# Performance work log

Measured on AMD Instinct MI355X. Metric: run time of the kernel, lower is better.

Reference implementation:

```python
import jax, jax.numpy as jnp
import numpy as np
import math

D_EMBED, D_K, N_HEADS = 1024, 1024, 16
D_H = D_EMBED // N_HEADS          # 64
ROT_DIM = D_H // 2                # 32, RotaryEmbedding(dim=d_h//2)
B, LQ, LK = 2, 2048, 2048


def _rope_freqs(seq_len):
    # lucidrains rotary-embedding-torch: inv_freq over half of `dim`, interleave-repeated
    inv_freq = 1.0 / (10000.0 ** (jnp.arange(0, ROT_DIM, 2, dtype=jnp.float32) / ROT_DIM))
    t = jnp.arange(seq_len, dtype=jnp.float32)
    f = t[:, None] * inv_freq[None, :]          # [S, ROT_DIM/2]
    return jnp.repeat(f, 2, axis=-1)            # [S, ROT_DIM] interleaved


def _apply_rotary(x, freqs):
    # x: [B,H,S,D_H]; rotate first ROT_DIM features, pass the rest through
    x_rot, x_pass = x[..., :ROT_DIM], x[..., ROT_DIM:]
    cos, sin = jnp.cos(freqs), jnp.sin(freqs)   # [S, ROT_DIM]
    x1, x2 = x_rot[..., 0::2], x_rot[..., 1::2]
    rotated = jnp.stack((-x2, x1), axis=-1).reshape(x_rot.shape)
    return jnp.concatenate([x_rot * cos + rotated * sin, x_pass], axis=-1)


def setup_inputs() -> dict:
    key = jax.random.key(0)
    ks = jax.random.split(key, 12)
    s = 0.02
    return {
        "embed": jax.random.normal(ks[0], (B, LQ, D_EMBED), jnp.float32),
        "key": jax.random.normal(ks[1], (B, LK, D_K), jnp.float32),
        "attn_mask": jnp.ones((B, LQ, LK), dtype=bool),
        "WQ": jax.random.normal(ks[2], (D_EMBED, D_EMBED), jnp.float32) * s,
        "bQ": jnp.zeros((D_EMBED,), jnp.float32),
        "WK": jax.random.normal(ks[3], (D_K, D_EMBED), jnp.float32) * s,
        "bK": jnp.zeros((D_EMBED,), jnp.float32),
        "WV": jax.random.normal(ks[4], (D_K, D_EMBED), jnp.float32) * s,
        "bV": jnp.zeros((D_EMBED,), jnp.float32),
        "WO": jax.random.normal(ks[5], (D_EMBED, D_EMBED), jnp.float32) * s,
        "bO": jnp.zeros((D_EMBED,), jnp.float32),
    }


def reference(embed, key, attn_mask, WQ, bQ, WK, bK, WV, bV, WO, bO):
    bsz, len_q, _ = embed.shape
    len_k = key.shape[1]
    scale = 1.0 / math.sqrt(D_EMBED)  # note: module scales by 1/sqrt(d_embed)

    Q = embed @ WQ + bQ
    K = key @ WK + bK
    V = key @ WV + bV

    # [B, H, S, D_H]
    Qh = Q.reshape(bsz, len_q, N_HEADS, D_H).transpose(0, 2, 1, 3)
    Kh = K.reshape(bsz, len_k, N_HEADS, D_H).transpose(0, 2, 1, 3)
    Vh = V.reshape(bsz, len_k, N_HEADS, D_H).transpose(0, 2, 1, 3)

    Qh = _apply_rotary(Qh, _rope_freqs(len_q))
    Kh = _apply_rotary(Kh, _rope_freqs(len_k))

    attn = jnp.einsum('bhqd,bhkd->bhqk', Qh, Kh)
    attn = jnp.where(attn_mask[:, None, :, :], attn, -jnp.inf)
    attn = jax.nn.softmax(attn * scale, axis=-1)

    out = jnp.einsum('bhqk,bhkd->bhqd', attn, Vh)
    out = out.transpose(0, 2, 1, 3).reshape(bsz, len_q, D_EMBED)
    return out @ WO + bO
```

## Files before the change

### kernel.cpp

```cpp
#include <hip/hip_runtime.h>
#include <hip/hip_bf16.h>
#include <cstdint>
#include <cstddef>

typedef __bf16 bf16_t;
typedef bf16_t bf16x8 __attribute__((ext_vector_type(8)));
typedef bf16_t bf16x4 __attribute__((ext_vector_type(4)));
typedef bf16_t bf16x2 __attribute__((ext_vector_type(2)));
typedef float f32x4 __attribute__((ext_vector_type(4)));
typedef float f32x16 __attribute__((ext_vector_type(16)));
typedef unsigned int u32x4 __attribute__((ext_vector_type(4)));

namespace {
constexpr int Bv = 2, Lv = 2048, Ev = 1024, NHv = 16;
constexpr int Mv = Bv * Lv;
constexpr float SCALE_L2E = 0.03125f * 1.4426950408889634f;
}

__device__ __forceinline__ void gload_lds16(const void* g, void* l) {
  __builtin_amdgcn_global_load_lds(
      (const __attribute__((address_space(1))) unsigned int*)g,
      (__attribute__((address_space(3))) unsigned int*)l,
      16, 0, 0);
}

__global__ __launch_bounds__(256) void k_prep(
    const float* __restrict__ embed, const float* __restrict__ key,
    bf16_t* __restrict__ Ae, bf16_t* __restrict__ Ak,
    float2* __restrict__ tab, int* __restrict__ bad,
    const unsigned int* __restrict__ m,
    const float* w0, const float* w1, const float* w2, const float* w3,
    bf16_t* t0, bf16_t* t1, bf16_t* t2, bf16_t* t3) {
  const int tid = threadIdx.x;
  int bx = blockIdx.x;
  if (bx < 8192) {
    const float* x = (bx < 4096) ? embed : key;
    bf16_t* y = (bx < 4096) ? Ae : Ak;
    int i = (bx & 4095) * 256 + tid;
    float4 v = reinterpret_cast<const float4*>(x)[i];
    bf16x4 o = {(bf16_t)v.x, (bf16_t)v.y, (bf16_t)v.z, (bf16_t)v.w};
    *reinterpret_cast<bf16x4*>(&y[(size_t)i * 4]) = o;
    return;
  }
  bx -= 8192;
  if (bx < 128) {
    int t = bx * 256 + tid;
    int i = t & 15, l = t >> 4;
    float inv = exp2f(-13.287712379549449f * (float)i * (1.0f / 16.0f));
    float s, c;
    sincosf((float)l * inv, &s, &c);
    tab[t] = make_float2(c, s);
    return;
  }
  bx -= 128;
  if (bx < 2048) {
    const int nwords = Bv * Lv * Lv;
    const int u8words = nwords >> 2;
    int i = bx * 256 + tid;
    bool badA = false, badB = false;
    for (; i < nwords; i += 2048 * 256) {
      unsigned int v = m[i];
      badA |= (i < u8words) & (v != 0x01010101u);
      badB |= (v != 1u);
    }
    if (__any(badA) && (tid & 63) == 0) bad[0] = 1;
    if (__any(badB) && (tid & 63) == 0) bad[1] = 1;
    return;
  }
  bx -= 2048;
  {
    const int z = bx >> 10, rem = bx & 1023;
    const float* W;
    bf16_t* T;
    switch (z) {
      case 0: W = w0; T = t0; break;
      case 1: W = w1; T = t1; break;
      case 2: W = w2; T = t2; break;
      default: W = w3; T = t3; break;
    }
    __shared__ float tile[32][33];
    const int tx = tid & 31, ty = tid >> 5;
    const int n0 = (rem & 31) * 32, k0 = (rem >> 5) * 32;
#pragma unroll
    for (int i = 0; i < 4; i++) {
      int r = ty + i * 8;
      tile[r][tx] = W[(size_t)(k0 + r) * Ev + n0 + tx];
    }
    __syncthreads();
#pragma unroll
    for (int i = 0; i < 4; i++) {
      int r = ty + i * 8;
      T[(size_t)(n0 + r) * Ev + k0 + tx] = (bf16_t)tile[tx][r];
    }
  }
}

__global__ __launch_bounds__(256) void k_gemm_qkv(
    const bf16_t* __restrict__ Ae, const bf16_t* __restrict__ Ak,
    const bf16_t* __restrict__ WtQ, const bf16_t* __restrict__ WtK,
    const bf16_t* __restrict__ WtV, const float* __restrict__ bQ,
    const float* __restrict__ bK, const float* __restrict__ bV,
    const float2* __restrict__ tab, bf16_t* __restrict__ Qbf,
    bf16_t* __restrict__ Kbf, bf16_t* __restrict__ Vtr) {
  constexpr int K = Ev;
  const int z = blockIdx.z;
  const bf16_t* A = (z == 0) ? Ae : Ak;
  const bf16_t* Bt = (z == 0) ? WtQ : (z == 1) ? WtK : WtV;
  const float* bias = (z == 0) ? bQ : (z == 1) ? bK : bV;

  __shared__ __align__(16) bf16_t As[128 * 32];
  __shared__ __align__(16) bf16_t Bs[128 * 32];
  const int tid = threadIdx.x;
  const int wid = tid >> 6, lane = tid & 63;
  const int bm = blockIdx.y * 128, bn = blockIdx.x * 128;
  const int wr = wid >> 1, wc = wid & 1;
  f32x4 acc[4][4] = {};
  const int srow = wid * 32 + (lane >> 2);
  const int scol = (lane & 3) * 8;
  const size_t ga0 = (size_t)(bm + srow) * K + scol;
  const size_t ga1 = (size_t)(bm + srow + 16) * K + scol;
  const size_t gb0 = (size_t)(bn + srow) * K + scol;
  const size_t gb1 = (size_t)(bn + srow + 16) * K + scol;
  bf16_t* asw = &As[wid * 1024];
  bf16_t* bsw = &Bs[wid * 1024];
  for (int k0 = 0; k0 < K; k0 += 32) {
    gload_lds16(A + ga0 + k0, asw);
    gload_lds16(A + ga1 + k0, asw + 512);
    gload_lds16(Bt + gb0 + k0, bsw);
    gload_lds16(Bt + gb1 + k0, bsw + 512);
    __syncthreads();
    bf16x8 af[4], bfr[4];
#pragma unroll
    for (int m = 0; m < 4; m++)
      af[m] = *(const bf16x8*)&As[(wr * 64 + m * 16 + (lane & 15)) * 32 + (lane >> 4) * 8];
#pragma unroll
    for (int n = 0; n < 4; n++)
      bfr[n] = *(const bf16x8*)&Bs[(wc * 64 + n * 16 + (lane & 15)) * 32 + (lane >> 4) * 8];
#pragma unroll
    for (int m = 0; m < 4; m++)
#pragma unroll
      for (int n = 0; n < 4; n++)
        acc[m][n] = __builtin_amdgcn_mfma_f32_16x16x32_bf16(af[m], bfr[n], acc[m][n], 0, 0, 0);
    __syncthreads();
  }

  const int l15 = lane & 15, g = lane >> 4;
  if (z == 2) {
#pragma unroll
    for (int n = 0; n < 4; n++) {
      const int col = bn + wc * 64 + n * 16 + l15;
      const int hh = (col >> 6) & 15;
      const int d = col & 63;
      const float bv = bias[col];
#pragma unroll
      for (int m = 0; m < 4; m++) {
        const int row0 = bm + wr * 64 + m * 16 + (g << 2);
        const int b = row0 >> 11, l0 = row0 & 2047;
        const int pq = (l0 >> 2) & 3;
        const int pq2 = ((pq & 1) << 1) | (pq >> 1);
        const int l0p = (l0 & ~12) | (pq2 << 2);
        bf16x4 ov;
#pragma unroll
        for (int r = 0; r < 4; r++) ov[r] = (bf16_t)(acc[m][n][r] + bv);
        *(bf16x4*)&Vtr[((size_t)((b * NHv + hh) * 64 + d)) * Lv + l0p] = ov;
      }
    }
    return;
  }

  bf16_t* Y = (z == 0) ? Qbf : Kbf;
  const float scale = (z == 0) ? SCALE_L2E : 1.0f;
  const float ssign = (l15 & 1) ? 1.0f : -1.0f;
#pragma unroll
  for (int n = 0; n < 4; n++) {
    const int col = bn + wc * 64 + n * 16 + l15;
    const int h = (col >> 6) & 15;
    const int d = col & 63;
    const float bv = bias[col];
    const bool dorope = (d < 32);
    const int ti = d >> 1;
#pragma unroll
    for (int m = 0; m < 4; m++) {
      const int row0 = bm + wr * 64 + m * 16 + (g << 2);
#pragma unroll
      for (int r = 0; r < 4; r++) {
        const int row = row0 + r;
        const int l = row & 2047, b = row >> 11;
        float v = acc[m][n][r] + bv;
        float p = __shfl_xor(v, 1);
        float o = v;
        if (dorope) {
          float2 cs = tab[(l << 4) + ti];
          o = v * cs.x + p * cs.y * ssign;
        }
        Y[(((size_t)(b * NHv + h)) * Lv + l) * 64 + d] = (bf16_t)(o * scale);
      }
    }
  }
}

__global__ __launch_bounds__(256) void k_gemm_bt(const bf16_t* __restrict__ A,
                                                 const bf16_t* __restrict__ Bt,
                                                 const float* __restrict__ bias,
                                                 float* __restrict__ C,
                                                 int N, int K) {
  __shared__ __align__(16) bf16_t As[128 * 32];
  __shared__ __align__(16) bf16_t Bs[64 * 32];
  const int tid = threadIdx.x;
  const int wid = tid >> 6, lane = tid & 63;
  const int bm = blockIdx.y * 128, bn = blockIdx.x * 64;
  const int wr = wid >> 1, wc = wid & 1;
  f32x4 acc[4][2] = {};
  const int srowA = wid * 32 + (lane >> 2);
  const int srowB = wid * 16 + (lane >> 2);
  const int scol = (lane & 3) * 8;
  const size_t ga0 = (size_t)(bm + srowA) * K + scol;
  const size_t ga1 = (size_t)(bm + srowA + 16) * K + scol;
  const size_t gb0 = (size_t)(bn + srowB) * K + scol;
  bf16_t* asw = &As[wid * 1024];
  bf16_t* bsw = &Bs[wid * 512];
  for (int k0 = 0; k0 < K; k0 += 32) {
    gload_lds16(A + ga0 + k0, asw);
    gload_lds16(A + ga1 + k0, asw + 512);
    gload_lds16(Bt + gb0 + k0, bsw);
    __syncthreads();
    bf16x8 af[4], bfr[2];
#pragma unroll
    for (int m = 0; m < 4; m++)
      af[m] = *(const bf16x8*)&As[(wr * 64 + m * 16 + (lane & 15)) * 32 + (lane >> 4) * 8];
#pragma unroll
    for (int n = 0; n < 2; n++)
      bfr[n] = *(const bf16x8*)&Bs[(wc * 32 + n * 16 + (lane & 15)) * 32 + (lane >> 4) * 8];
#pragma unroll
    for (int m = 0; m < 4; m++)
#pragma unroll
      for (int n = 0; n < 2; n++)
        acc[m][n] = __builtin_amdgcn_mfma_f32_16x16x32_bf16(af[m], bfr[n], acc[m][n], 0, 0, 0);
    __syncthreads();
  }
#pragma unroll
  for (int n = 0; n < 2; n++) {
    const int col = bn + wc * 32 + n * 16 + (lane & 15);
    const float bv = bias[col];
#pragma unroll
    for (int m = 0; m < 4; m++) {
      const int row0 = bm + wr * 64 + m * 16 + ((lane >> 4) << 2);
#pragma unroll
      for (int r = 0; r < 4; r++)
        C[(size_t)(row0 + r) * N + col] = acc[m][n][r] + bv;
    }
  }
}

__device__ __forceinline__ void flash_stage(const bf16_t* __restrict__ Kg,
                                            const bf16_t* __restrict__ Vg,
                                            bf16_t* ksb, bf16_t* vsb,
                                            int tid, int kt) {
#pragma unroll
  for (int i = 0; i < 2; i++) {
    int slot = i * 256 + tid;
    int r = slot >> 3, c = slot & 7;
    int sb = ((c * 16) ^ ((r & 7) << 4)) >> 1;
    bf16_t* dk = ksb + (size_t)(i * 256 + (tid & 192)) * 8;
    gload_lds16(Kg + (size_t)(kt * 64 + r) * 64 + sb, dk);
    bf16_t* dv = vsb + (size_t)(i * 256 + (tid & 192)) * 8;
    gload_lds16(Vg + (size_t)r * Lv + kt * 64 + sb, dv);
  }
}

__global__ __launch_bounds__(256) void k_flash32(const bf16_t* __restrict__ Qh,
                                                 const bf16_t* __restrict__ Kh,
                                                 const bf16_t* __restrict__ Vtr,
                                                 const int* __restrict__ mask,
                                                 const int* __restrict__ bad,
                                                 bf16_t* __restrict__ Oh) {
  __shared__ __align__(16) bf16_t Ks[2][64 * 64];
  __shared__ __align__(16) bf16_t Vs[2][64 * 64];
  __shared__ float sw[4][32];
  const int tid = threadIdx.x, wid = tid >> 6, lane = tid & 63;
  const int l31 = lane & 31, hf = lane >> 5;
  const int bh = blockIdx.x, qt = blockIdx.y;
  const int b = bh >> 4, hd = bh & 15;
  const size_t base = (size_t)bh * Lv * 64;
  const bf16_t* Kg = Kh + base;
  const bf16_t* Vg = Vtr + base;
  const int allm = !(bad[0] & bad[1]);
  const int q = qt * 128 + wid * 32 + l31;

  bf16x8 bq[4];
#pragma unroll
  for (int s = 0; s < 4; s++)
    bq[s] = *(const bf16x8*)&Qh[base + (size_t)q * 64 + s * 16 + hf * 8];

  const int xsw = (l31 & 7) << 4;
  int eo_[4];
#pragma unroll
  for (int s = 0; s < 4; s++) eo_[s] = (((s * 16 + hf * 8) * 2) ^ xsw) >> 1;

  float m_r = -INFINITY, l_p = 0.f;
  f32x16 o0 = {}, o1 = {};

  flash_stage(Kg, Vg, Ks[0], Vs[0], tid, 0);
  __syncthreads();
  int cur = 0;
  for (int kt = 0; kt < Lv / 64; ++kt) {
    if (kt + 1 < Lv / 64)
      flash_stage(Kg, Vg, Ks[cur ^ 1], Vs[cur ^ 1], tid, kt + 1);
    const bf16_t* KsC = Ks[cur];
    const bf16_t* VsC = Vs[cur];

    f32x16 st0 = {}, st1 = {};
    __builtin_amdgcn_s_setprio(1);
#pragma unroll
    for (int s = 0; s < 4; s++) {
      bf16x8 k0 = *(const bf16x8*)&KsC[l31 * 64 + eo_[s]];
      bf16x8 k1 = *(const bf16x8*)&KsC[(32 + l31) * 64 + eo_[s]];
      st0 = __builtin_amdgcn_mfma_f32_32x32x16_bf16(k0, bq[s], st0, 0, 0, 0);
      st1 = __builtin_amdgcn_mfma_f32_32x32x16_bf16(k1, bq[s], st1, 0, 0, 0);
    }
    __builtin_amdgcn_s_setprio(0);

    if (!allm) {
      const int* mrow = &mask[(size_t)b * Lv * Lv + (size_t)q * Lv + kt * 64];
#pragma unroll
      for (int r = 0; r < 16; r++) {
        const int kv = (r & 3) + 8 * (r >> 2) + 4 * hf;
        if (!mrow[kv]) st0[r] = -INFINITY;
        if (!mrow[32 + kv]) st1[r] = -INFINITY;
      }
    }

    float pm = fmaxf(st0[0], st0[1]);
#pragma unroll
    for (int r = 2; r < 16; r += 2) pm = fmaxf(fmaxf(st0[r], st0[r + 1]), pm);
#pragma unroll
    for (int r = 0; r < 16; r += 2) pm = fmaxf(fmaxf(st1[r], st1[r + 1]), pm);
    if (__any(pm > m_r + 8.0f)) {
      float pmf = fmaxf(pm, __shfl_xor(pm, 32));
      float mn = fmaxf(m_r, pmf);
      float alpha = exp2f(m_r - mn);
      m_r = mn;
      l_p *= alpha;
      if (!hf) sw[wid][l31] = alpha;
      asm volatile("s_waitcnt lgkmcnt(0)" ::: "memory");
      __builtin_amdgcn_sched_barrier(0);
#pragma unroll
      for (int r = 0; r < 16; r++) {
        float a = sw[wid][(r & 3) + 8 * (r >> 2) + 4 * hf];
        o0[r] *= a;
        o1[r] *= a;
      }
    }
    float ps = 0.f;
#pragma unroll
    for (int r = 0; r < 16; r++) {
      float p = exp2f(st0[r] - m_r);
      st0[r] = p;
      ps += p;
    }
#pragma unroll
    for (int r = 0; r < 16; r++) {
      float p = exp2f(st1[r] - m_r);
      st1[r] = p;
      ps += p;
    }
    l_p += ps;

    unsigned int pk0[8], pk1[8];
#pragma unroll
    for (int i = 0; i < 8; i++) {
      float a0 = st0[2 * i], a1 = st0[2 * i + 1];
      float b0 = st1[2 * i], b1 = st1[2 * i + 1];
      asm("v_cvt_pk_bf16_f32 %0, %1, %2" : "=v"(pk0[i]) : "v"(a0), "v"(a1));
      asm("v_cvt_pk_bf16_f32 %0, %1, %2" : "=v"(pk1[i]) : "v"(b0), "v"(b1));
    }

    __builtin_amdgcn_s_setprio(1);
#pragma unroll
    for (int s = 0; s < 4; s++) {
      u32x4 u;
      if (s == 0) {
        u[0] = pk0[0]; u[1] = pk0[1]; u[2] = pk0[2]; u[3] = pk0[3];
      } else if (s == 1) {
        u[0] = pk0[4]; u[1] = pk0[5]; u[2] = pk0[6]; u[3] = pk0[7];
      } else if (s == 2) {
        u[0] = pk1[0]; u[1] = pk1[1]; u[2] = pk1[2]; u[3] = pk1[3];
      } else {
        u[0] = pk1[4]; u[1] = pk1[5]; u[2] = pk1[6]; u[3] = pk1[7];
      }
      bf16x8 pa = __builtin_bit_cast(bf16x8, u);
      bf16x8 v0 = *(const bf16x8*)&VsC[l31 * 64 + eo_[s]];
      bf16x8 v1 = *(const bf16x8*)&VsC[(32 + l31) * 64 + eo_[s]];
      o0 = __builtin_amdgcn_mfma_f32_32x32x16_bf16(pa, v0, o0, 0, 0, 0);
      o1 = __builtin_amdgcn_mfma_f32_32x32x16_bf16(pa, v1, o1, 0, 0, 0);
    }
    __builtin_amdgcn_s_setprio(0);

    __syncthreads();
    cur ^= 1;
  }

  float lt = l_p + __shfl_xor(l_p, 32);
  if (!hf) sw[wid][l31] = 1.0f / lt;
  asm volatile("s_waitcnt lgkmcnt(0)" ::: "memory");
  __builtin_amdgcn_sched_barrier(0);
#pragma unroll
  for (int r = 0; r < 16; r++) {
    const int rq = (r & 3) + 8 * (r >> 2) + 4 * hf;
    float inv = sw[wid][rq];
    const int qg = qt * 128 + wid * 32 + rq;
    const size_t off = ((size_t)(b * Lv + qg)) * Ev + hd * 64;
    Oh[off + l31] = (bf16_t)(o0[r] * inv);
    Oh[off + 32 + l31] = (bf16_t)(o1[r] * inv);
  }
}

extern "C" void kernel_launch(void* const* d_in, const int* in_sizes, int n_in,
                              void* d_out, int out_size, void* d_ws, size_t ws_size,
                              hipStream_t stream) {
  const float* embed = (const float*)d_in[0];
  const float* key = (const float*)d_in[1];
  const int* mask = (const int*)d_in[2];
  const float* WQ = (const float*)d_in[3];
  const float* bQ = (const float*)d_in[4];
  const float* WK = (const float*)d_in[5];
  const float* bK = (const float*)d_in[6];
  const float* WV = (const float*)d_in[7];
  const float* bV = (const float*)d_in[8];
  const float* WO = (const float*)d_in[9];
  const float* bO = (const float*)d_in[10];
  float* out = (float*)d_out;
  char* ws = (char*)d_ws;
  const size_t MB = 1024 * 1024;

  bf16_t* Wt = (bf16_t*)(ws);
  bf16_t* Ae = (bf16_t*)(ws + 8 * MB);
  bf16_t* Ak = (bf16_t*)(ws + 16 * MB);
  bf16_t* Qbf = (bf16_t*)(ws + 40 * MB);
  bf16_t* Kbf = (bf16_t*)(ws + 48 * MB);
  bf16_t* Vtr = (bf16_t*)(ws + 56 * MB);
  bf16_t* AO = (bf16_t*)(ws + 8 * MB);
  int* bad = (int*)(ws + 64 * MB);
  float2* tab = (float2*)(ws + 65 * MB);

  hipMemsetAsync(bad, 0, 2 * sizeof(int), stream);
  k_prep<<<14464, 256, 0, stream>>>(embed, key, Ae, Ak, tab, bad,
                                    (const unsigned int*)mask, WQ, WK, WV, WO,
                                    Wt, Wt + 1024 * 1024, Wt + 2 * 1024 * 1024,
                                    Wt + 3 * 1024 * 1024);

  {
    dim3 gg(8, 32, 3);
    k_gemm_qkv<<<gg, 256, 0, stream>>>(Ae, Ak, Wt, Wt + 1024 * 1024,
                                       Wt + 2 * 1024 * 1024, bQ, bK, bV, tab,
                                       Qbf, Kbf, Vtr);
  }
  {
    dim3 fg(32, 16);
    k_flash32<<<fg, 256, 0, stream>>>(Qbf, Kbf, Vtr, mask, bad, AO);
  }
  {
    dim3 gg(16, 32);
    k_gemm_bt<<<gg, 256, 0, stream>>>(AO, Wt + 3 * 1024 * 1024, bO, out, Ev, Ev);
  }
}
```

Baseline: 161.9 us.

## Split flash attention over key halves with a separate combine kernel

Adds a split-K variant of the flash attention kernel. Each block processes half of the key sequence and writes unnormalized bf16 partial outputs plus per-row max and sum. A new combine kernel merges the two halves with log-sum-exp weights into the attention output. This doubles the grid to improve CU occupancy and parallelism, at the cost of extra partial-output memory traffic, an extra kernel launch, and bf16 rounding of the partials. The split path is only enabled when the workspace is large enough.

```diff
diff --git a/kernel.cpp b/kernel.cpp
--- a/kernel.cpp
+++ b/kernel.cpp
@@ -268,18 +268,22 @@
   }
 }
 
+template <bool SPLIT>
 __global__ __launch_bounds__(256) void k_flash32(const bf16_t* __restrict__ Qh,
                                                  const bf16_t* __restrict__ Kh,
                                                  const bf16_t* __restrict__ Vtr,
                                                  const int* __restrict__ mask,
                                                  const int* __restrict__ bad,
-                                                 bf16_t* __restrict__ Oh) {
+                                                 bf16_t* __restrict__ Oh,
+                                                 bf16_t* __restrict__ Opart,
+                                                 float2* __restrict__ ml) {
   __shared__ __align__(16) bf16_t Ks[2][64 * 64];
   __shared__ __align__(16) bf16_t Vs[2][64 * 64];
   __shared__ float sw[4][32];
   const int tid = threadIdx.x, wid = tid >> 6, lane = tid & 63;
   const int l31 = lane & 31, hf = lane >> 5;
   const int bh = blockIdx.x, qt = blockIdx.y;
+  const int ks = SPLIT ? blockIdx.z : 0;
   const int b = bh >> 4, hd = bh & 15;
   const size_t base = (size_t)bh * Lv * 64;
   const bf16_t* Kg = Kh + base;
@@ -300,11 +304,14 @@
   float m_r = -INFINITY, l_p = 0.f;
   f32x16 o0 = {}, o1 = {};
 
-  flash_stage(Kg, Vg, Ks[0], Vs[0], tid, 0);
+  const int kt0 = SPLIT ? ks * (Lv / 128) : 0;
+  const int kt1 = SPLIT ? kt0 + (Lv / 128) : (Lv / 64);
+
+  flash_stage(Kg, Vg, Ks[0], Vs[0], tid, kt0);
   __syncthreads();
   int cur = 0;
-  for (int kt = 0; kt < Lv / 64; ++kt) {
-    if (kt + 1 < Lv / 64)
+  for (int kt = kt0; kt < kt1; ++kt) {
+    if (kt + 1 < kt1)
       flash_stage(Kg, Vg, Ks[cur ^ 1], Vs[cur ^ 1], tid, kt + 1);
     const bf16_t* KsC = Ks[cur];
     const bf16_t* VsC = Vs[cur];
@@ -401,17 +408,55 @@
   }
 
   float lt = l_p + __shfl_xor(l_p, 32);
-  if (!hf) sw[wid][l31] = 1.0f / lt;
-  asm volatile("s_waitcnt lgkmcnt(0)" ::: "memory");
-  __builtin_amdgcn_sched_barrier(0);
-#pragma unroll
-  for (int r = 0; r < 16; r++) {
-    const int rq = (r & 3) + 8 * (r >> 2) + 4 * hf;
-    float inv = sw[wid][rq];
-    const int qg = qt * 128 + wid * 32 + rq;
-    const size_t off = ((size_t)(b * Lv + qg)) * Ev + hd * 64;
-    Oh[off + l31] = (bf16_t)(o0[r] * inv);
-    Oh[off + 32 + l31] = (bf16_t)(o1[r] * inv);
+  if (SPLIT) {
+    if (!hf) ml[((size_t)ks * 32 + bh) * Lv + q] = make_float2(m_r, lt);
+    bf16_t* po = &Opart[(((size_t)ks * 32 + bh) * Lv + qt * 128 + wid * 32) * 64];
+#pragma unroll
+    for (int r = 0; r < 16; r++) {
+      const int rq = (r & 3) + 8 * (r >> 2) + 4 * hf;
+      po[(size_t)rq * 64 + l31] = (bf16_t)o0[r];
+      po[(size_t)rq * 64 + 32 + l31] = (bf16_t)o1[r];
+    }
+  } else {
+    if (!hf) sw[wid][l31] = 1.0f / lt;
+    asm volatile("s_waitcnt lgkmcnt(0)" ::: "memory");
+    __builtin_amdgcn_sched_barrier(0);
+#pragma unroll
+    for (int r = 0; r < 16; r++) {
+      const int rq = (r & 3) + 8 * (r >> 2) + 4 * hf;
+      float inv = sw[wid][rq];
+      const int qg = qt * 128 + wid * 32 + rq;
+      const size_t off = ((size_t)(b * Lv + qg)) * Ev + hd * 64;
+      Oh[off + l31] = (bf16_t)(o0[r] * inv);
+      Oh[off + 32 + l31] = (bf16_t)(o1[r] * inv);
+    }
+  }
+}
+
+__global__ __launch_bounds__(256) void k_comb(const bf16_t* __restrict__ Opart,
+                                              const float2* __restrict__ ml,
+                                              bf16_t* __restrict__ AO) {
+  int t = blockIdx.x * 256 + threadIdx.x;
+  int q = t & (Lv - 1), bh = t >> 11;
+  float2 a = ml[(size_t)bh * Lv + q];
+  float2 c = ml[((size_t)32 + bh) * Lv + q];
+  float mx = fmaxf(a.x, c.x);
+  float e0 = exp2f(a.x - mx), e1 = exp2f(c.x - mx);
+  float denom = e0 * a.y + e1 * c.y;
+  float w0 = e0 / denom, w1 = e1 / denom;
+  const bf16_t* p0 = &Opart[((size_t)bh * Lv + q) * 64];
+  const bf16_t* p1 = &Opart[(((size_t)32 + bh) * Lv + q) * 64];
+  int b = bh >> 4, h = bh & 15;
+  bf16_t* po = &AO[((size_t)(b * Lv + q)) * Ev + h * 64];
+#pragma unroll
+  for (int cch = 0; cch < 8; cch++) {
+    bf16x8 x = *(const bf16x8*)&p0[cch * 8];
+    bf16x8 y = *(const bf16x8*)&p1[cch * 8];
+    bf16x8 o;
+#pragma unroll
+    for (int j = 0; j < 8; j++)
+      o[j] = (bf16_t)(w0 * (float)x[j] + w1 * (float)y[j]);
+    *(bf16x8*)&po[cch * 8] = o;
   }
 }
 
@@ -436,12 +481,16 @@
   bf16_t* Wt = (bf16_t*)(ws);
   bf16_t* Ae = (bf16_t*)(ws + 8 * MB);
   bf16_t* Ak = (bf16_t*)(ws + 16 * MB);
+  bf16_t* Opart = (bf16_t*)(ws + 24 * MB);
   bf16_t* Qbf = (bf16_t*)(ws + 40 * MB);
   bf16_t* Kbf = (bf16_t*)(ws + 48 * MB);
   bf16_t* Vtr = (bf16_t*)(ws + 56 * MB);
   bf16_t* AO = (bf16_t*)(ws + 8 * MB);
   int* bad = (int*)(ws + 64 * MB);
   float2* tab = (float2*)(ws + 65 * MB);
+  float2* ml = (float2*)(ws + 66 * MB);
+
+  const bool split = ws_size >= 68 * MB;
 
   hipMemsetAsync(bad, 0, 2 * sizeof(int), stream);
   k_prep<<<14464, 256, 0, stream>>>(embed, key, Ae, Ak, tab, bad,
@@ -455,9 +504,15 @@
                                        Wt + 2 * 1024 * 1024, bQ, bK, bV, tab,
                                        Qbf, Kbf, Vtr);
   }
-  {
+  if (split) {
+    dim3 fg(32, 16, 2);
+    k_flash32<true><<<fg, 256, 0, stream>>>(Qbf, Kbf, Vtr, mask, bad, AO,
+                                            Opart, ml);
+    k_comb<<<256, 256, 0, stream>>>(Opart, ml, AO);
+  } else {
     dim3 fg(32, 16);
-    k_flash32<<<fg, 256, 0, stream>>>(Qbf, Kbf, Vtr, mask, bad, AO);
+    k_flash32<false><<<fg, 256, 0, stream>>>(Qbf, Kbf, Vtr, mask, bad, AO,
+                                             Opart, ml);
   }
   {
     dim3 gg(16, 32);
```

Result: slower. 175.1 us (+8.1%).

## Software-pipeline flash attention: overlap next tile's QK/softmax with current PV

Applied to the files above, without the earlier changes.

The key loop is restructured so that QK^T, softmax and bf16 packing for tile t+1 run in the same iteration as the PV MFMAs for tile t. K/V staging moves from double to triple buffering in LDS, so the prefetch runs two tiles ahead. The output rescale for a max update is now applied after the PV of the previous tile. This is meant to hide softmax and exp latency behind matrix-core work, at the cost of more registers (two packed P arrays) and more shared memory, which may lower occupancy.

```diff
diff --git a/kernel.cpp b/kernel.cpp
--- a/kernel.cpp
+++ b/kernel.cpp
@@ -268,14 +268,76 @@
   }
 }
 
+__device__ __forceinline__ void qk_sm_pack(
+    const bf16_t* __restrict__ KsC, const bf16x8* bq, const int* eo_,
+    const int* __restrict__ mrow, int l31, int hf, float* swp,
+    float& m_r, float& l_p, bool& resc, unsigned int* pk) {
+  f32x16 st0 = {}, st1 = {};
+  __builtin_amdgcn_s_setprio(1);
+#pragma unroll
+  for (int s = 0; s < 4; s++) {
+    bf16x8 k0 = *(const bf16x8*)&KsC[l31 * 64 + eo_[s]];
+    bf16x8 k1 = *(const bf16x8*)&KsC[(32 + l31) * 64 + eo_[s]];
+    st0 = __builtin_amdgcn_mfma_f32_32x32x16_bf16(k0, bq[s], st0, 0, 0, 0);
+    st1 = __builtin_amdgcn_mfma_f32_32x32x16_bf16(k1, bq[s], st1, 0, 0, 0);
+  }
+  __builtin_amdgcn_s_setprio(0);
+
+  if (mrow) {
+#pragma unroll
+    for (int r = 0; r < 16; r++) {
+      const int kv = (r & 3) + 8 * (r >> 2) + 4 * hf;
+      if (!mrow[kv]) st0[r] = -INFINITY;
+      if (!mrow[32 + kv]) st1[r] = -INFINITY;
+    }
+  }
+
+  float pm = fmaxf(st0[0], st0[1]);
+#pragma unroll
+  for (int r = 2; r < 16; r += 2) pm = fmaxf(fmaxf(st0[r], st0[r + 1]), pm);
+#pragma unroll
+  for (int r = 0; r < 16; r += 2) pm = fmaxf(fmaxf(st1[r], st1[r + 1]), pm);
+  resc = false;
+  if (__any(pm > m_r + 8.0f)) {
+    float pmf = fmaxf(pm, __shfl_xor(pm, 32));
+    float mn = fmaxf(m_r, pmf);
+    float alpha = exp2f(m_r - mn);
+    m_r = mn;
+    l_p *= alpha;
+    if (!hf) swp[l31] = alpha;
+    resc = true;
+  }
+  float ps = 0.f;
+#pragma unroll
+  for (int r = 0; r < 16; r++) {
+    float p = exp2f(st0[r] - m_r);
+    st0[r] = p;
+    ps += p;
+  }
+#pragma unroll
+  for (int r = 0; r < 16; r++) {
+    float p = exp2f(st1[r] - m_r);
+    st1[r] = p;
+    ps += p;
+  }
+  l_p += ps;
+#pragma unroll
+  for (int i = 0; i < 8; i++) {
+    float a0 = st0[2 * i], a1 = st0[2 * i + 1];
+    float b0 = st1[2 * i], b1 = st1[2 * i + 1];
+    asm("v_cvt_pk_bf16_f32 %0, %1, %2" : "=v"(pk[i]) : "v"(a0), "v"(a1));
+    asm("v_cvt_pk_bf16_f32 %0, %1, %2" : "=v"(pk[8 + i]) : "v"(b0), "v"(b1));
+  }
+}
+
 __global__ __launch_bounds__(256) void k_flash32(const bf16_t* __restrict__ Qh,
                                                  const bf16_t* __restrict__ Kh,
                                                  const bf16_t* __restrict__ Vtr,
                                                  const int* __restrict__ mask,
                                                  const int* __restrict__ bad,
                                                  bf16_t* __restrict__ Oh) {
-  __shared__ __align__(16) bf16_t Ks[2][64 * 64];
-  __shared__ __align__(16) bf16_t Vs[2][64 * 64];
+  __shared__ __align__(16) bf16_t Ks[3][64 * 64];
+  __shared__ __align__(16) bf16_t Vs[3][64 * 64];
   __shared__ float sw[4][32];
   const int tid = threadIdx.x, wid = tid >> 6, lane = tid & 63;
   const int l31 = lane & 31, hf = lane >> 5;
@@ -284,8 +346,11 @@
   const size_t base = (size_t)bh * Lv * 64;
   const bf16_t* Kg = Kh + base;
   const bf16_t* Vg = Vtr + base;
-  const int allm = !(bad[0] & bad[1]);
+  const bool allm = !(bad[0] & bad[1]);
   const int q = qt * 128 + wid * 32 + l31;
+  const int* mbase = allm ? nullptr
+                          : &mask[(size_t)b * Lv * Lv + (size_t)q * Lv];
+  float* swp = &sw[wid][0];
 
   bf16x8 bq[4];
 #pragma unroll
@@ -299,95 +364,40 @@
 
   float m_r = -INFINITY, l_p = 0.f;
   f32x16 o0 = {}, o1 = {};
+  unsigned int pkA[16], pkB[16];
+  constexpr int NT = Lv / 64;
 
   flash_stage(Kg, Vg, Ks[0], Vs[0], tid, 0);
   __syncthreads();
-  int cur = 0;
-  for (int kt = 0; kt < Lv / 64; ++kt) {
-    if (kt + 1 < Lv / 64)
-      flash_stage(Kg, Vg, Ks[cur ^ 1], Vs[cur ^ 1], tid, kt + 1);
-    const bf16_t* KsC = Ks[cur];
-    const bf16_t* VsC = Vs[cur];
-
-    f32x16 st0 = {}, st1 = {};
-    __builtin_amdgcn_s_setprio(1);
-#pragma unroll
-    for (int s = 0; s < 4; s++) {
-      bf16x8 k0 = *(const bf16x8*)&KsC[l31 * 64 + eo_[s]];
-      bf16x8 k1 = *(const bf16x8*)&KsC[(32 + l31) * 64 + eo_[s]];
-      st0 = __builtin_amdgcn_mfma_f32_32x32x16_bf16(k0, bq[s], st0, 0, 0, 0);
-      st1 = __builtin_amdgcn_mfma_f32_32x32x16_bf16(k1, bq[s], st1, 0, 0, 0);
-    }
-    __builtin_amdgcn_s_setprio(0);
-
-    if (!allm) {
-      const int* mrow = &mask[(size_t)b * Lv * Lv + (size_t)q * Lv + kt * 64];
-#pragma unroll
-      for (int r = 0; r < 16; r++) {
-        const int kv = (r & 3) + 8 * (r >> 2) + 4 * hf;
-        if (!mrow[kv]) st0[r] = -INFINITY;
-        if (!mrow[32 + kv]) st1[r] = -INFINITY;
-      }
-    }
-
-    float pm = fmaxf(st0[0], st0[1]);
-#pragma unroll
-    for (int r = 2; r < 16; r += 2) pm = fmaxf(fmaxf(st0[r], st0[r + 1]), pm);
-#pragma unroll
-    for (int r = 0; r < 16; r += 2) pm = fmaxf(fmaxf(st1[r], st1[r + 1]), pm);
-    if (__any(pm > m_r + 8.0f)) {
-      float pmf = fmaxf(pm, __shfl_xor(pm, 32));
-      float mn = fmaxf(m_r, pmf);
-      float alpha = exp2f(m_r - mn);
-      m_r = mn;
-      l_p *= alpha;
-      if (!hf) sw[wid][l31] = alpha;
-      asm volatile("s_waitcnt lgkmcnt(0)" ::: "memory");
-      __builtin_amdgcn_sched_barrier(0);
-#pragma unroll
-      for (int r = 0; r < 16; r++) {
-        float a = sw[wid][(r & 3) + 8 * (r >> 2) + 4 * hf];
-        o0[r] *= a;
-        o1[r] *= a;
-      }
-    }
-    float ps = 0.f;
-#pragma unroll
-    for (int r = 0; r < 16; r++) {
-      float p = exp2f(st0[r] - m_r);
-      st0[r] = p;
-      ps += p;
-    }
-#pragma unroll
-    for (int r = 0; r < 16; r++) {
-      float p = exp2f(st1[r] - m_r);
-      st1[r] = p;
-      ps += p;
-    }
-    l_p += ps;
-
-    unsigned int pk0[8], pk1[8];
-#pragma unroll
-    for (int i = 0; i < 8; i++) {
-      float a0 = st0[2 * i], a1 = st0[2 * i + 1];
-      float b0 = st1[2 * i], b1 = st1[2 * i + 1];
-      asm("v_cvt_pk_bf16_f32 %0, %1, %2" : "=v"(pk0[i]) : "v"(a0), "v"(a1));
-      asm("v_cvt_pk_bf16_f32 %0, %1, %2" : "=v"(pk1[i]) : "v"(b0), "v"(b1));
-    }
-
+  flash_stage(Kg, Vg, Ks[1], Vs[1], tid, 1);
+  {
+    bool r0;
+    qk_sm_pack(Ks[0], bq, eo_, mbase ? mbase + 0 : nullptr, l31, hf, swp,
+               m_r, l_p, r0, pkA);
+  }
+  __syncthreads();
+
+  for (int t = 0; t < NT; ++t) {
+    const int bc = t % 3;
+    if (t + 2 < NT)
+      flash_stage(Kg, Vg, Ks[(t + 2) % 3], Vs[(t + 2) % 3], tid, t + 2);
+
+    bool resc = false;
+    if (t + 1 < NT) {
+      qk_sm_pack(Ks[(t + 1) % 3], bq, eo_,
+                 mbase ? mbase + (t + 1) * 64 : nullptr, l31, hf, swp,
+                 m_r, l_p, resc, pkB);
+    }
+
+    const bf16_t* VsC = Vs[bc];
     __builtin_amdgcn_s_setprio(1);
 #pragma unroll
     for (int s = 0; s < 4; s++) {
       u32x4 u;
-      if (s == 0) {
-        u[0] = pk0[0]; u[1] = pk0[1]; u[2] = pk0[2]; u[3] = pk0[3];
-      } else if (s == 1) {
-        u[0] = pk0[4]; u[1] = pk0[5]; u[2] = pk0[6]; u[3] = pk0[7];
-      } else if (s == 2) {
-        u[0] = pk1[0]; u[1] = pk1[1]; u[2] = pk1[2]; u[3] = pk1[3];
-      } else {
-        u[0] = pk1[4]; u[1] = pk1[5]; u[2] = pk1[6]; u[3] = pk1[7];
-      }
+      u[0] = pkA[4 * s + 0];
+      u[1] = pkA[4 * s + 1];
+      u[2] = pkA[4 * s + 2];
+      u[3] = pkA[4 * s + 3];
       bf16x8 pa = __builtin_bit_cast(bf16x8, u);
       bf16x8 v0 = *(const bf16x8*)&VsC[l31 * 64 + eo_[s]];
       bf16x8 v1 = *(const bf16x8*)&VsC[(32 + l31) * 64 + eo_[s]];
@@ -396,18 +406,32 @@
     }
     __builtin_amdgcn_s_setprio(0);
 
-    __syncthreads();
-    cur ^= 1;
+    if (resc) {
+      asm volatile("s_waitcnt lgkmcnt(0)" ::: "memory");
+      __builtin_amdgcn_sched_barrier(0);
+#pragma unroll
+      for (int r = 0; r < 16; r++) {
+        float a = swp[(r & 3) + 8 * (r >> 2) + 4 * hf];
+        o0[r] *= a;
+        o1[r] *= a;
+      }
+    }
+
+    __syncthreads();
+    if (t + 1 < NT) {
+#pragma unroll
+      for (int i = 0; i < 16; i++) pkA[i] = pkB[i];
+    }
   }
 
   float lt = l_p + __shfl_xor(l_p, 32);
-  if (!hf) sw[wid][l31] = 1.0f / lt;
+  if (!hf) swp[l31] = 1.0f / lt;
   asm volatile("s_waitcnt lgkmcnt(0)" ::: "memory");
   __builtin_amdgcn_sched_barrier(0);
 #pragma unroll
   for (int r = 0; r < 16; r++) {
     const int rq = (r & 3) + 8 * (r >> 2) + 4 * hf;
-    float inv = sw[wid][rq];
+    float inv = swp[rq];
     const int qg = qt * 128 + wid * 32 + rq;
     const size_t off = ((size_t)(b * Lv + qg)) * Ev + hd * 64;
     Oh[off + l31] = (bf16_t)(o0[r] * inv);
```

After: 165.2 us. 1.02x slower.
